# Optimization experiments

Measured on AMD Instinct MI355X. Metric: run time of the kernel, lower is better.

## Reference

```python
import jax, jax.numpy as jnp
import numpy as np


def ternarize(w):
    """TWN ternarization: delta=0.7*mean|w|, alpha = mean of |w| over kept entries."""
    aw = jnp.abs(w)
    delta = 0.7 * jnp.mean(aw)
    mask = (aw > delta).astype(w.dtype)
    alpha = jnp.sum(aw * mask) / jnp.maximum(jnp.sum(mask), 1.0)
    return alpha * jnp.sign(w) * mask


def conv3x3(x, w):
    # NCHW input, OIHW weight, stride 1, padding 1
    return jax.lax.conv_general_dilated(
        x, w, window_strides=(1, 1), padding=((1, 1), (1, 1)),
        dimension_numbers=("NCHW", "OIHW", "NCHW"))


def maxpool2(x):
    return jax.lax.reduce_window(
        x, -jnp.inf, jax.lax.max,
        window_dimensions=(1, 1, 2, 2), window_strides=(1, 1, 2, 2),
        padding="VALID")


def setup_inputs() -> dict:
    key = jax.random.key(0)
    ks = jax.random.split(key, 9)
    B = 4096
    return {
        "x":   jax.random.normal(ks[0], (B, 3, 32, 32), dtype=jnp.float32),
        "w1":  jax.random.normal(ks[1], (16, 3, 3, 3), dtype=jnp.float32) * 0.1,
        "b1":  jax.random.normal(ks[2], (16,), dtype=jnp.float32) * 0.01,
        "w2":  jax.random.normal(ks[3], (32, 16, 3, 3), dtype=jnp.float32) * 0.1,
        "b2":  jax.random.normal(ks[4], (32,), dtype=jnp.float32) * 0.01,
        "wf1": jax.random.normal(ks[5], (128, 32 * 8 * 8), dtype=jnp.float32) * 0.05,
        "bf1": jax.random.normal(ks[6], (128,), dtype=jnp.float32) * 0.01,
        "wf2": jax.random.normal(ks[7], (10, 128), dtype=jnp.float32) * 0.05,
        "bf2": jax.random.normal(ks[8], (10,), dtype=jnp.float32) * 0.01,
    }


def reference(x, w1, b1, w2, b2, wf1, bf1, wf2, bf2):
    h = jax.nn.relu(conv3x3(x, ternarize(w1)) + b1[None, :, None, None])
    h = maxpool2(h)                                    # [B,16,16,16]
    h = jax.nn.relu(conv3x3(h, ternarize(w2)) + b2[None, :, None, None])
    h = maxpool2(h)                                    # [B,32,8,8]
    h = h.reshape(-1, 32 * 8 * 8)
    h = jax.nn.relu(h @ ternarize(wf1).T + bf1)        # [B,128]
    return h @ ternarize(wf2).T + bf2                  # [B,10]
```

## Files before the change

kernel.cpp:

```cpp
#include <hip/hip_runtime.h>
#include <math.h>


typedef _Float16 half2v __attribute__((ext_vector_type(2)));
typedef _Float16 half4  __attribute__((ext_vector_type(4)));
typedef _Float16 half8  __attribute__((ext_vector_type(8)));
typedef float    f32x4  __attribute__((ext_vector_type(4)));
typedef unsigned u32x2  __attribute__((ext_vector_type(2)));

#define WF1_N 262144
#define WF1_SLICES 64
#define WF1_SLICE 4096

__device__ __forceinline__ float block_reduce_256(float v, float* red, int t) {
    red[t] = v; __syncthreads();
    for (int o = 128; o > 0; o >>= 1) {
        if (t < o) red[t] += red[t + o];
        __syncthreads();
    }
    float r = red[0]; __syncthreads();
    return r;
}

__device__ __forceinline__ float wave_sum64(float v) {
#pragma unroll
    for (int o = 32; o > 0; o >>= 1) v += __shfl_xor(v, o);
    return v;
}

__device__ __forceinline__ unsigned pk16(float a, float b) {
    half2v h;
    h[0] = (_Float16)a;
    h[1] = (_Float16)b;
    return __builtin_bit_cast(unsigned, h);
}

__global__ void tern_stageA(const float* __restrict__ w1,
                            const float* __restrict__ w2,
                            const float* __restrict__ wf1,
                            const float* __restrict__ wf2,
                            _Float16* __restrict__ tw1f,
                            _Float16* __restrict__ tw2f,
                            float* __restrict__ twf2,
                            float* __restrict__ part_sum) {
    __shared__ float red[256];
    const int t = threadIdx.x;
    const int bid = blockIdx.x;

    if (bid < WF1_SLICES) {
        const float4* src = reinterpret_cast<const float4*>(wf1 + (size_t)bid * WF1_SLICE);
        float s = 0.f;
#pragma unroll
        for (int j = 0; j < 4; ++j) {
            const float4 v = src[t + j * 256];
            s += fabsf(v.x) + fabsf(v.y) + fabsf(v.z) + fabsf(v.w);
        }
        const float tot = block_reduce_256(s, red, t);
        if (t == 0) part_sum[bid] = tot;
        return;
    }

    const float* w;
    int n;
    const int which = bid - WF1_SLICES;
    switch (which) {
        case 0: w = w1;  n = 432;  break;
        case 1: w = w2;  n = 4608; break;
        default: w = wf2; n = 1280; break;
    }
    float s = 0.f;
    for (int i = t; i < n; i += 256) s += fabsf(w[i]);
    const float delta = 0.7f * block_reduce_256(s, red, t) / (float)n;
    float sa = 0.f, cnt = 0.f;
    for (int i = t; i < n; i += 256) {
        float a = fabsf(w[i]);
        if (a > delta) { sa += a; cnt += 1.f; }
    }
    const float tot_sa = block_reduce_256(sa, red, t);
    const float tot_cnt = block_reduce_256(cnt, red, t);
    const float alpha = tot_sa / fmaxf(tot_cnt, 1.0f);

    switch (which) {
        case 0:
            for (int o = t; o < 768; o += 256) {
                int j = o & 3;
                int l = (o >> 2) & 63;
                int m = o >> 8;
                int rho = m * 4 + (l >> 4);
                int co = l & 15;
                float v = 0.f;
                if (rho < 9 && j < 3) {
                    float wv = w1[co * 27 + (rho / 3) * 9 + (rho % 3) * 3 + j];
                    v = (fabsf(wv) > delta) ? copysignf(alpha, wv) : 0.f;
                }
                tw1f[o] = (_Float16)v;
            }
            break;
        case 1:
            for (int o = t; o < 4608; o += 256) {
                int j  = o & 3;
                int ll = (o >> 2) & 63;
                int nt = (o >> 8) & 1;
                int s9 = o >> 9;
                int ci = (ll >> 4) * 4 + j;
                int co = (ll & 15) + nt * 16;
                float wv = w2[(co * 16 + ci) * 9 + s9];
                float v = (fabsf(wv) > delta) ? copysignf(alpha, wv) : 0.f;
                tw2f[o] = (_Float16)v;
            }
            break;
        default:
            for (int o = t; o < 1280; o += 256) {
                float wv = wf2[o];
                twf2[o] = (fabsf(wv) > delta) ? copysignf(alpha, wv) : 0.f;
            }
            break;
    }
}

__global__ void tern_stageB(const float* __restrict__ wf1,
                            const float* __restrict__ part_sum,
                            float* __restrict__ part_sa,
                            float* __restrict__ part_cnt,
                            _Float16* __restrict__ twf1) {
    __shared__ float red[256];
    const int t = threadIdx.x;
    const int bid = blockIdx.x;

    float v = (t < WF1_SLICES) ? part_sum[t] : 0.f;
    const float delta = 0.7f * block_reduce_256(v, red, t) / (float)WF1_N;

    const float4* src = reinterpret_cast<const float4*>(wf1 + (size_t)bid * WF1_SLICE);
    float sa = 0.f, cnt = 0.f;
#pragma unroll
    for (int j = 0; j < 4; ++j) {
        const float4 w4 = src[t + j * 256];
        half4 hv;
        float a;
        a = fabsf(w4.x); if (a > delta) { sa += a; cnt += 1.f; }
        hv[0] = (_Float16)((fabsf(w4.x) > delta) ? copysignf(1.0f, w4.x) : 0.f);
        a = fabsf(w4.y); if (a > delta) { sa += a; cnt += 1.f; }
        hv[1] = (_Float16)((fabsf(w4.y) > delta) ? copysignf(1.0f, w4.y) : 0.f);
        a = fabsf(w4.z); if (a > delta) { sa += a; cnt += 1.f; }
        hv[2] = (_Float16)((fabsf(w4.z) > delta) ? copysignf(1.0f, w4.z) : 0.f);
        a = fabsf(w4.w); if (a > delta) { sa += a; cnt += 1.f; }
        hv[3] = (_Float16)((fabsf(w4.w) > delta) ? copysignf(1.0f, w4.w) : 0.f);
        const int o = bid * WF1_SLICE + (t + j * 256) * 4;
        const int n = o >> 11, k = o & 2047;
        const int dst = ((k >> 5) << 12) + ((n >> 4) << 9) +
                        (((k >> 3) & 3) << 7) + ((n & 15) << 3) + (k & 7);
        *reinterpret_cast<half4*>(twf1 + dst) = hv;
    }
    const float tot_sa = block_reduce_256(sa, red, t);
    const float tot_cnt = block_reduce_256(cnt, red, t);
    if (t == 0) { part_sa[bid] = tot_sa; part_cnt[bid] = tot_cnt; }
}

#define H1P 18
#define PSZ 3472
#define H1SZ (18*18*H1P)

__global__ __launch_bounds__(256, 5)
void conv12_kernel(const float* __restrict__ x,
                   const float* __restrict__ b1,
                   const float* __restrict__ b2,
                   const _Float16* __restrict__ tw1f,
                   const _Float16* __restrict__ tw2f,
                   _Float16* __restrict__ h2p) {
    __shared__ __align__(16) _Float16 PA[PSZ];
    __shared__ __align__(16) _Float16 PB[PSZ];
    __shared__ __align__(16) _Float16 h1s[H1SZ];
    __shared__ __align__(16) _Float16 h2s[2048];
    __shared__ float b1s[16], b2s[32];

    const int t = threadIdx.x;
    const int b = blockIdx.x;
    const int wid = t >> 6, l = t & 63;

    float4 xv4[3];
    {
        const float4* xb4 = reinterpret_cast<const float4*>(x + (size_t)b * 3072);
#pragma unroll
        for (int j = 0; j < 3; ++j) xv4[j] = xb4[t + j * 256];
    }
    half4 bfr1[3];
#pragma unroll
    for (int m = 0; m < 3; ++m)
        bfr1[m] = *reinterpret_cast<const half4*>(tw1f + (size_t)(m * 64 + l) * 4);
    if (t < 16) b1s[t] = b1[t];
    if (t < 32) b2s[t] = b2[t];

    {
        const float4 z = {0.f, 0.f, 0.f, 0.f};
        float4* pa4 = reinterpret_cast<float4*>(PA);
        float4* pb4 = reinterpret_cast<float4*>(PB);
        float4* h14 = reinterpret_cast<float4*>(h1s);
        for (int i = t; i < PSZ * 2 / 16; i += 256) { pa4[i] = z; pb4[i] = z; }
        for (int i = t; i < H1SZ * 2 / 16; i += 256) h14[i] = z;
    }
    __syncthreads();

    {
#pragma unroll
        for (int j = 0; j < 3; ++j) {
            const int f = t + j * 256;
            const int c = f >> 8, rem = f & 255;
            const int iy = rem >> 3, ix = (rem & 7) << 2;
            const int idx = ((c * 34) + iy + 1) * 34 + 1 + ix;
            const float4 v = xv4[j];
            const unsigned w0 = __builtin_bit_cast(unsigned, __builtin_amdgcn_cvt_pkrtz(v.x, v.y));
            const unsigned w1 = __builtin_bit_cast(unsigned, __builtin_amdgcn_cvt_pkrtz(v.z, v.w));
            const half2v h0 = __builtin_bit_cast(half2v, w0);
            const half2v h1 = __builtin_bit_cast(half2v, w1);
            *reinterpret_cast<unsigned*>(&PB[idx - 1]) = w0;
            *reinterpret_cast<unsigned*>(&PB[idx + 1]) = w1;
            PA[idx] = h0[0];
            *reinterpret_cast<unsigned*>(&PA[idx + 1]) = (w0 >> 16) | (w1 << 16);
            PA[idx + 3] = h1[1];
        }
    }
    __syncthreads();

    {
        const int r15 = l & 15, g = l >> 4;
        const int p = r15 & 1;
        int laneIdx[3];
#pragma unroll
        for (int m = 0; m < 3; ++m) {
            int rho = m * 4 + g;
            if (rho > 8) rho = 0;
            const int c = rho / 3, ky = rho % 3;
            laneIdx[m] = ((c * 34 + ky) * 34 + r15 - p) >> 1;
        }
        const unsigned* basep = p ? reinterpret_cast<const unsigned*>(PB)
                                  : reinterpret_cast<const unsigned*>(PA);
        const float bia = b1s[r15];

#pragma unroll 1
        for (int i = 0; i < 8; ++i) {
            const int P = wid * 8 + i;
            const int py = P >> 1, xh = P & 1;
            const int x0 = xh * 16;
            f32x4 accA = {0.f, 0.f, 0.f, 0.f};
            f32x4 accB = {0.f, 0.f, 0.f, 0.f};
#pragma unroll
            for (int h2 = 0; h2 < 2; ++h2) {
                const int y = 2 * py + h2;
                const int uoff = (y * 34 + x0) >> 1;
                f32x4 acc = {0.f, 0.f, 0.f, 0.f};
#pragma unroll
                for (int m = 0; m < 3; ++m) {
                    const unsigned* q = basep + laneIdx[m] + uoff;
                    u32x2 d;
                    d.x = q[0];
                    d.y = q[1];
                    const half4 a = __builtin_bit_cast(half4, d);
                    acc = __builtin_amdgcn_mfma_f32_16x16x16f16(a, bfr1[m], acc, 0, 0, 0);
                }
                if (h2 == 0) accA = acc; else accB = acc;
            }
            float e0 = fmaxf(fmaxf(accA[0], accA[1]), fmaxf(accB[0], accB[1]));
            float e1 = fmaxf(fmaxf(accA[2], accA[3]), fmaxf(accB[2], accB[3]));
            e0 = fmaxf(e0 + bia, 0.f);
            e1 = fmaxf(e1 + bia, 0.f);
            const int px0 = xh * 8 + g * 2;
            const int pix = (py + 1) * 18 + (px0 + 1);
            h1s[pix * H1P + r15]       = (_Float16)e0;
            h1s[(pix + 1) * H1P + r15] = (_Float16)e1;
        }
    }

    half4 bfr[9][2];
#pragma unroll
    for (int s = 0; s < 9; ++s)
#pragma unroll
        for (int nt = 0; nt < 2; ++nt)
            bfr[s][nt] = *reinterpret_cast<const half4*>(
                tw2f + (size_t)((s * 2 + nt) * 64 + l) * 4);
    __syncthreads();

    {
        const int xq = l & 15, g = l >> 4;
        const unsigned* h1u = reinterpret_cast<const unsigned*>(h1s);
        float sav[2][2];
#pragma unroll
        for (int yy = 0; yy < 4; ++yy) {
            const int y = wid * 4 + yy;
            const unsigned* qb = h1u + (y * 18 + xq) * 9 + g * 2;
            f32x4 acc0 = {0.f, 0.f, 0.f, 0.f};
            f32x4 acc1 = {0.f, 0.f, 0.f, 0.f};
#pragma unroll
            for (int s = 0; s < 9; ++s) {
                const int dy = s / 3, dx = s % 3;
                const int off = (dy * 18 + dx) * 9;
                u32x2 d;
                d.x = qb[off];
                d.y = qb[off + 1];
                const half4 a = __builtin_bit_cast(half4, d);
                acc0 = __builtin_amdgcn_mfma_f32_16x16x16f16(a, bfr[s][0], acc0, 0, 0, 0);
                acc1 = __builtin_amdgcn_mfma_f32_16x16x16f16(a, bfr[s][1], acc1, 0, 0, 0);
            }
            const float p00 = fmaxf(acc0[0], acc0[1]);
            const float p01 = fmaxf(acc0[2], acc0[3]);
            const float p10 = fmaxf(acc1[0], acc1[1]);
            const float p11 = fmaxf(acc1[2], acc1[3]);
            if ((yy & 1) == 0) {
                sav[0][0] = p00; sav[0][1] = p01;
                sav[1][0] = p10; sav[1][1] = p11;
            } else {
                const int py = (wid * 4 + yy) >> 1;
                const float v00 = fmaxf(fmaxf(sav[0][0], p00) + b2s[xq], 0.f);
                const float v01 = fmaxf(fmaxf(sav[0][1], p01) + b2s[xq], 0.f);
                const float v10 = fmaxf(fmaxf(sav[1][0], p10) + b2s[xq + 16], 0.f);
                const float v11 = fmaxf(fmaxf(sav[1][1], p11) + b2s[xq + 16], 0.f);
                unsigned* h2u = reinterpret_cast<unsigned*>(h2s);
                h2u[xq * 32 + py * 4 + g]        = pk16(v00, v01);
                h2u[(xq + 16) * 32 + py * 4 + g] = pk16(v10, v11);
            }
        }
    }
    __syncthreads();

    {
        const float4 v = reinterpret_cast<const float4*>(h2s)[t];
        reinterpret_cast<float4*>(h2p + (size_t)b * 2048)[t] = v;
    }
}

#define FC_PAD 8

__global__ __launch_bounds__(1024, 2)
void fc_kernel(const _Float16* __restrict__ h2p,
               const _Float16* __restrict__ twf1,
               const float* __restrict__ part_sa,
               const float* __restrict__ part_cnt,
               const float* __restrict__ bf1,
               const float* __restrict__ twf2,
               const float* __restrict__ bf2,
               float* __restrict__ out) {
    __shared__ __align__(16) _Float16 As[16][1024 + FC_PAD];
    __shared__ float red[4][3][2][256];
    __shared__ float Hs[16][132];

    const int t = threadIdx.x;
    const int wid = t >> 6, l = t & 63;
    const int kq = wid & 3, ng = wid >> 2;
    const int lx = l & 15, g = l >> 4;
    const int m0 = blockIdx.x * 16;

    const float alphaW = wave_sum64(part_sa[l]) / fmaxf(wave_sum64(part_cnt[l]), 1.0f);

    f32x4 acc[2];
    acc[0] = (f32x4){0.f, 0.f, 0.f, 0.f};
    acc[1] = (f32x4){0.f, 0.f, 0.f, 0.f};

    const int stg_r = t >> 7;
    const int stg_c = (t & 127) * 8;

#pragma unroll
    for (int h = 0; h < 2; ++h) {
        if (h) __syncthreads();
#pragma unroll
        for (int p = 0; p < 2; ++p) {
            const int r = stg_r + p * 8;
            *reinterpret_cast<float4*>(&As[r][stg_c]) =
                *reinterpret_cast<const float4*>(
                    h2p + (size_t)(m0 + r) * 2048 + h * 1024 + stg_c);
        }
        __syncthreads();
#pragma unroll
        for (int it = 0; it < 8; ++it) {
            const int kk = kq * 256 + it * 32;
            const int kc = (h * 1024 + kk) >> 5;
            const half8 a = *reinterpret_cast<const half8*>(&As[lx][kk + g * 8]);
#pragma unroll
            for (int nt = 0; nt < 2; ++nt) {
                const half8 bb = *reinterpret_cast<const half8*>(
                    twf1 + ((size_t)kc << 12) + ((ng * 2 + nt) << 9) + l * 8);
                acc[nt] = __builtin_amdgcn_mfma_f32_16x16x32_f16(a, bb, acc[nt], 0, 0, 0);
            }
        }
    }

    if (kq != 0) {
#pragma unroll
        for (int nt = 0; nt < 2; ++nt)
            *reinterpret_cast<f32x4*>(&red[ng][kq - 1][nt][l * 4]) = acc[nt];
    }
    __syncthreads();
    if (kq == 0) {
#pragma unroll
        for (int nt = 0; nt < 2; ++nt) {
#pragma unroll
            for (int q = 0; q < 3; ++q)
                acc[nt] += *reinterpret_cast<const f32x4*>(&red[ng][q][nt][l * 4]);
            const int col = ng * 32 + nt * 16 + lx;
            const float bias = bf1[col];
#pragma unroll
            for (int r = 0; r < 4; ++r)
                Hs[g * 4 + r][col] = fmaxf(acc[nt][r] * alphaW + bias, 0.f);
        }
    }
    __syncthreads();

    if (t < 160) {
        const int m = t / 10, n = t % 10;
        float a = bf2[n];
#pragma unroll 8
        for (int k = 0; k < 128; ++k) a += Hs[m][k] * twf2[n * 128 + k];
        out[(size_t)(m0 + m) * 10 + n] = a;
    }
}

extern "C" void kernel_launch(void* const* d_in, const int* in_sizes, int n_in,
                              void* d_out, int out_size, void* d_ws, size_t ws_size,
                              hipStream_t stream) {
    const float* x   = (const float*)d_in[0];
    const float* w1  = (const float*)d_in[1];
    const float* b1  = (const float*)d_in[2];
    const float* w2  = (const float*)d_in[3];
    const float* b2  = (const float*)d_in[4];
    const float* wf1 = (const float*)d_in[5];
    const float* bf1 = (const float*)d_in[6];
    const float* wf2 = (const float*)d_in[7];
    const float* bf2 = (const float*)d_in[8];
    float* out = (float*)d_out;
    const int B = in_sizes[0] / (3 * 32 * 32);

    char* ws = (char*)d_ws;
    _Float16*  tw1f  = (_Float16*)(ws + 0);
    _Float16*  tw2f  = (_Float16*)(ws + 1536);
    _Float16*  twf1  = (_Float16*)(ws + 10752);
    float*     twf2  = (float*)(ws + 535040);
    _Float16*  h2p   = (_Float16*)(ws + 540160);
    float*     part_sum = (float*)(ws + 17317376);
    float*     part_sa  = part_sum + 64;
    float*     part_cnt = part_sa + 64;

    tern_stageA<<<WF1_SLICES + 3, 256, 0, stream>>>(w1, w2, wf1, wf2,
                                                    tw1f, tw2f, twf2, part_sum);
    tern_stageB<<<WF1_SLICES, 256, 0, stream>>>(wf1, part_sum, part_sa, part_cnt, twf1);
    conv12_kernel<<<B, 256, 0, stream>>>(x, b1, b2, tw1f, tw2f, h2p);
    fc_kernel<<<B / 16, 1024, 0, stream>>>(h2p, twf1, part_sa, part_cnt,
                                           bf1, twf2, bf2, out);
}
```

Measured before the change: 62.61 us.

## Process two images per conv block and overlap second image staging with conv2

The conv kernel now handles two batch images per block, launching half as many blocks. The zero-initialisation of padded shared buffers and the conv2 weight fragment loads are amortised over two images. The second image's global load is issued during conv1 of the first image, and its staging into LDS overlaps conv2 of the first. This trades parallelism (fewer blocks) and extra live registers for lower per-image setup cost and better latency hiding.

Measured after the change: 66.61 us. 1.06x slower.

```diff
diff --git a/kernel.cpp b/kernel.cpp
--- a/kernel.cpp
+++ b/kernel.cpp
@@ -174,12 +174,12 @@
     __shared__ float b1s[16], b2s[32];
 
     const int t = threadIdx.x;
-    const int b = blockIdx.x;
+    const int b0 = blockIdx.x * 2;
     const int wid = t >> 6, l = t & 63;
 
     float4 xv4[3];
     {
-        const float4* xb4 = reinterpret_cast<const float4*>(x + (size_t)b * 3072);
+        const float4* xb4 = reinterpret_cast<const float4*>(x + (size_t)b0 * 3072);
 #pragma unroll
         for (int j = 0; j < 3; ++j) xv4[j] = xb4[t + j * 256];
     }
@@ -198,16 +198,15 @@
         for (int i = t; i < PSZ * 2 / 16; i += 256) { pa4[i] = z; pb4[i] = z; }
         for (int i = t; i < H1SZ * 2 / 16; i += 256) h14[i] = z;
     }
-    __syncthreads();
-
-    {
+
+    auto stage_x = [&](const float4* xv) {
 #pragma unroll
         for (int j = 0; j < 3; ++j) {
             const int f = t + j * 256;
             const int c = f >> 8, rem = f & 255;
             const int iy = rem >> 3, ix = (rem & 7) << 2;
             const int idx = ((c * 34) + iy + 1) * 34 + 1 + ix;
-            const float4 v = xv4[j];
+            const float4 v = xv[j];
             const unsigned w0 = __builtin_bit_cast(unsigned, __builtin_amdgcn_cvt_pkrtz(v.x, v.y));
             const unsigned w1 = __builtin_bit_cast(unsigned, __builtin_amdgcn_cvt_pkrtz(v.z, v.w));
             const half2v h0 = __builtin_bit_cast(half2v, w0);
@@ -218,24 +217,23 @@
             *reinterpret_cast<unsigned*>(&PA[idx + 1]) = (w0 >> 16) | (w1 << 16);
             PA[idx + 3] = h1[1];
         }
-    }
-    __syncthreads();
-
-    {
-        const int r15 = l & 15, g = l >> 4;
-        const int p = r15 & 1;
-        int laneIdx[3];
-#pragma unroll
-        for (int m = 0; m < 3; ++m) {
-            int rho = m * 4 + g;
-            if (rho > 8) rho = 0;
-            const int c = rho / 3, ky = rho % 3;
-            laneIdx[m] = ((c * 34 + ky) * 34 + r15 - p) >> 1;
-        }
-        const unsigned* basep = p ? reinterpret_cast<const unsigned*>(PB)
-                                  : reinterpret_cast<const unsigned*>(PA);
+    };
+
+    const int r15 = l & 15, g = l >> 4;
+    const int p = r15 & 1;
+    int laneIdx[3];
+#pragma unroll
+    for (int m = 0; m < 3; ++m) {
+        int rho = m * 4 + g;
+        if (rho > 8) rho = 0;
+        const int c = rho / 3, ky = rho % 3;
+        laneIdx[m] = ((c * 34 + ky) * 34 + r15 - p) >> 1;
+    }
+    const unsigned* basep = p ? reinterpret_cast<const unsigned*>(PB)
+                              : reinterpret_cast<const unsigned*>(PA);
+
+    auto do_conv1 = [&]() {
         const float bia = b1s[r15];
-
 #pragma unroll 1
         for (int i = 0; i < 8; ++i) {
             const int P = wid * 8 + i;
@@ -268,19 +266,11 @@
             h1s[pix * H1P + r15]       = (_Float16)e0;
             h1s[(pix + 1) * H1P + r15] = (_Float16)e1;
         }
-    }
+    };
 
     half4 bfr[9][2];
-#pragma unroll
-    for (int s = 0; s < 9; ++s)
-#pragma unroll
-        for (int nt = 0; nt < 2; ++nt)
-            bfr[s][nt] = *reinterpret_cast<const half4*>(
-                tw2f + (size_t)((s * 2 + nt) * 64 + l) * 4);
-    __syncthreads();
-
-    {
-        const int xq = l & 15, g = l >> 4;
+    auto do_conv2 = [&]() {
+        const int xq = r15;
         const unsigned* h1u = reinterpret_cast<const unsigned*>(h1s);
         float sav[2][2];
 #pragma unroll
@@ -318,13 +308,45 @@
                 h2u[(xq + 16) * 32 + py * 4 + g] = pk16(v10, v11);
             }
         }
-    }
-    __syncthreads();
-
-    {
+    };
+
+    auto do_write = [&](int b) {
         const float4 v = reinterpret_cast<const float4*>(h2s)[t];
         reinterpret_cast<float4*>(h2p + (size_t)b * 2048)[t] = v;
-    }
+    };
+
+    __syncthreads();
+    stage_x(xv4);
+    __syncthreads();
+
+    float4 yv4[3];
+    {
+        const float4* yb4 = reinterpret_cast<const float4*>(x + (size_t)(b0 + 1) * 3072);
+#pragma unroll
+        for (int j = 0; j < 3; ++j) yv4[j] = yb4[t + j * 256];
+    }
+
+    do_conv1();
+#pragma unroll
+    for (int s = 0; s < 9; ++s)
+#pragma unroll
+        for (int nt = 0; nt < 2; ++nt)
+            bfr[s][nt] = *reinterpret_cast<const half4*>(
+                tw2f + (size_t)((s * 2 + nt) * 64 + l) * 4);
+    __syncthreads();
+
+    do_conv2();
+    stage_x(yv4);
+    __syncthreads();
+
+    do_write(b0);
+    do_conv1();
+    __syncthreads();
+
+    do_conv2();
+    __syncthreads();
+
+    do_write(b0 + 1);
 }
 
 #define FC_PAD 8
@@ -440,7 +462,7 @@
     tern_stageA<<<WF1_SLICES + 3, 256, 0, stream>>>(w1, w2, wf1, wf2,
                                                     tw1f, tw2f, twf2, part_sum);
     tern_stageB<<<WF1_SLICES, 256, 0, stream>>>(wf1, part_sum, part_sa, part_cnt, twf1);
-    conv12_kernel<<<B, 256, 0, stream>>>(x, b1, b2, tw1f, tw2f, h2p);
+    conv12_kernel<<<B / 2, 256, 0, stream>>>(x, b1, b2, tw1f, tw2f, h2p);
     fc_kernel<<<B / 16, 1024, 0, stream>>>(h2p, twf1, part_sa, part_cnt,
                                            bf1, twf2, bf2, out);
 }
```
